# Optimization experiments

Measured on AMD Instinct MI355X. Metric: run time of the kernel, lower is better.

## Reference

```python
import jax, jax.numpy as jnp
import numpy as np

D_MODEL = 1024
NUM_HEADS = 16
MAX_SEQ_LEN = 2048
THETA = 10000.0
HEAD_DIM = D_MODEL // NUM_HEADS  # 64


def _trunc_normal(key, shape, std):
    # truncated normal in [-3, 3] sigma, matching nn.init.trunc_normal_
    return std * jax.random.truncated_normal(key, -3.0, 3.0, shape, dtype=jnp.float32)


def setup_inputs() -> dict:
    key = jax.random.key(0)
    kx, kq, kk, kv, ko = jax.random.split(key, 5)
    B, L = 2, 2048
    sigma = np.sqrt(2.0 / (D_MODEL + D_MODEL))
    x = jax.random.normal(kx, (B, L, D_MODEL), dtype=jnp.float32)
    token_positions = jnp.arange(L, dtype=jnp.int64 if jax.config.jax_enable_x64 else jnp.int32)[None, :]
    return {
        "x": x,
        "wq": _trunc_normal(kq, (D_MODEL, D_MODEL), sigma),
        "wk": _trunc_normal(kk, (D_MODEL, D_MODEL), sigma),
        "wv": _trunc_normal(kv, (D_MODEL, D_MODEL), sigma),
        "wo": _trunc_normal(ko, (D_MODEL, D_MODEL), sigma),
        "token_positions": token_positions,
    }


def _rope_tables():
    pos = jnp.arange(MAX_SEQ_LEN, dtype=jnp.float32)
    d_idx = jnp.arange(HEAD_DIM // 2, dtype=jnp.float32)
    inv_freq = THETA ** (-2.0 * d_idx / HEAD_DIM)
    angles = pos[:, None] * inv_freq[None, :]  # [max_seq_len, head_dim/2]
    return jnp.cos(angles), jnp.sin(angles)


def _apply_rope(x, cos, sin):
    # x: [b, n, l, h]; cos/sin: [1, l, h/2] (broadcast over b, n)
    xe = x[..., 0::2]
    xo = x[..., 1::2]
    oe = cos * xe - sin * xo
    oo = sin * xe + cos * xo
    # interleave back: stack last axis then flatten pairs
    out = jnp.stack([oe, oo], axis=-1)
    return out.reshape(x.shape)


def reference(x, wq, wk, wv, wo, token_positions):
    B, L, _ = x.shape
    cos_t, sin_t = _rope_tables()
    cos = cos_t[token_positions]  # [1, L, h/2]
    sin = sin_t[token_positions]

    def proj(w):
        y = jnp.einsum('bld,ed->ble', x, w)
        return y.reshape(B, L, NUM_HEADS, HEAD_DIM).transpose(0, 2, 1, 3)  # b n l h

    q, k, v = proj(wq), proj(wk), proj(wv)
    q = _apply_rope(q, cos, sin)
    k = _apply_rope(k, cos, sin)

    scale = 1.0 / np.sqrt(HEAD_DIM).astype(np.float32)
    logits = jnp.einsum('bnqh,bnkh->bnqk', q, k) * scale
    causal = jnp.tril(jnp.ones((L, L), dtype=bool))
    logits = jnp.where(causal[None, None], logits, -jnp.inf)
    scores = jax.nn.softmax(logits, axis=-1)
    out = jnp.einsum('bnqk,bnkh->bnqh', scores, v)
    out = out.transpose(0, 2, 1, 3).reshape(B, L, D_MODEL)
    return jnp.einsum('bld,ed->ble', out, wo)
```

## Files before the change

kernel.cpp:

```cpp
#include <hip/hip_runtime.h>
#include <stdint.h>
#include <stddef.h>

#define SEQ   2048
#define HD    64
#define DM    1024
#define NHEAD 16

typedef __bf16 bf16x8 __attribute__((ext_vector_type(8)));
typedef __bf16 bf16x4 __attribute__((ext_vector_type(4)));
typedef float  f32x4  __attribute__((ext_vector_type(4)));
typedef uint32_t u32x2 __attribute__((ext_vector_type(2)));
typedef uint32_t u32x4 __attribute__((ext_vector_type(4)));

#define MFMA16x16(a, b, c) __builtin_amdgcn_mfma_f32_16x16x32_bf16((a), (b), (c), 0, 0, 0)

__device__ __forceinline__ void gload16(const void* g, void* lds_uniform) {
    __builtin_amdgcn_global_load_lds(
        (const __attribute__((address_space(1))) uint32_t*)g,
        (__attribute__((address_space(3))) uint32_t*)lds_uniform, 16, 0, 0);
}

__global__ void prep_kernel(const float* __restrict__ x,
                            const float* __restrict__ wq, const float* __restrict__ wk,
                            const float* __restrict__ wv, const float* __restrict__ wo,
                            __bf16* __restrict__ xb, __bf16* __restrict__ wqkv,
                            __bf16* __restrict__ wob, float2* __restrict__ ctst) {
    int bid = blockIdx.x;
    if (bid < 4096) {
        int i = (bid * 256 + threadIdx.x) * 4;
        const float4 v = *(const float4*)(x + i);
        __bf16 o[4] = {(__bf16)v.x, (__bf16)v.y, (__bf16)v.z, (__bf16)v.w};
        *(uint64_t*)(xb + i) = *(const uint64_t*)o;
    } else if (bid < 8192) {
        int g = (bid - 4096) >> 10;
        int i = (((bid - 4096) & 1023) * 256 + threadIdx.x) * 4;
        const float* src = (g == 0) ? wq : (g == 1) ? wk : (g == 2) ? wv : wo;
        __bf16* dst = (g == 3) ? wob : (wqkv + (size_t)g * 1048576);
        const float4 v = *(const float4*)(src + i);
        __bf16 o[4] = {(__bf16)v.x, (__bf16)v.y, (__bf16)v.z, (__bf16)v.w};
        *(uint64_t*)(dst + i) = *(const uint64_t*)o;
    } else {
        int i = (bid - 8192) * 256 + threadIdx.x;
        int p = i & 31;
        int pos = i >> 5;
        float freq = expf(-(float)p * (logf(10000.0f) / 32.0f));
        float ang = (float)pos * freq;
        ctst[i] = make_float2(cosf(ang), sinf(ang));
    }
}

template <int MODE, int BN, int WPEU>
__global__ __launch_bounds__(256, WPEU)
void gemm_bt_kernel(const __bf16* __restrict__ A, const __bf16* __restrict__ W,
                    float* __restrict__ C, __bf16* __restrict__ Qb,
                    __bf16* __restrict__ Kb, __bf16* __restrict__ VTb,
                    const int* __restrict__ tpos, const float2* __restrict__ ctst,
                    int N, int K) {
    constexpr int NJ = BN >> 5;
    __shared__ __align__(16) char smem[16384 + BN * 128];
    char* As = smem;
    char* Bs = smem + 16384;
    const int lane = threadIdx.x & 63;
    const int w    = threadIdx.x >> 6;

    const int nbn = N / BN;
    const int per = (nbn * 32) >> 3;
    const int id  = blockIdx.x;
    const int lin = (id & 7) * per + (id >> 3);
    const int bm  = lin / nbn;
    const int bn  = lin % nbn;

    const int rbase = (w >> 1) * 64;
    const int cbase = (w & 1) * (BN / 2);

    f32x4 acc[4][NJ] = {};

    const int kt_iters = K >> 6;
    for (int kt = 0; kt < kt_iters; ++kt) {
        #pragma unroll
        for (int c = 0; c < 4; ++c) {
            int id2 = (c * 4 + w) * 64 + lane;
            int row = id2 >> 3, cc = id2 & 7;
            int koff = kt * 64 + ((cc ^ (row & 7)) << 3);
            gload16(A + (size_t)(bm * 128 + row) * K + koff, As + (c * 4 + w) * 1024);
        }
        #pragma unroll
        for (int c = 0; c < NJ; ++c) {
            int id2 = (c * 4 + w) * 64 + lane;
            int row = id2 >> 3, cc = id2 & 7;
            int koff = kt * 64 + ((cc ^ (row & 7)) << 3);
            gload16(W + (size_t)(bn * BN + row) * K + koff, Bs + (c * 4 + w) * 1024);
        }
        __syncthreads();
        #pragma unroll
        for (int ks = 0; ks < 2; ++ks) {
            bf16x8 af[4], bfr[NJ];
            #pragma unroll
            for (int i = 0; i < 4; ++i) {
                int row = rbase + i * 16 + (lane & 15);
                int c = ks * 4 + (lane >> 4);
                af[i] = *(const bf16x8*)(As + row * 128 + ((c ^ (row & 7)) << 4));
            }
            #pragma unroll
            for (int j = 0; j < NJ; ++j) {
                int row = cbase + j * 16 + (lane & 15);
                int c = ks * 4 + (lane >> 4);
                bfr[j] = *(const bf16x8*)(Bs + row * 128 + ((c ^ (row & 7)) << 4));
            }
            #pragma unroll
            for (int i = 0; i < 4; ++i)
                #pragma unroll
                for (int j = 0; j < NJ; ++j)
                    acc[i][j] = MFMA16x16(af[i], bfr[j], acc[i][j]);
        }
        __syncthreads();
    }

    if (MODE == 1) {
        #pragma unroll
        for (int i = 0; i < 4; ++i)
            #pragma unroll
            for (int j = 0; j < NJ; ++j)
                #pragma unroll
                for (int r = 0; r < 4; ++r) {
                    int m = bm * 128 + rbase + i * 16 + (lane >> 4) * 4 + r;
                    int n = bn * BN + cbase + j * 16 + (lane & 15);
                    C[(size_t)m * N + n] = acc[i][j][r];
                }
    } else {
        const int which = bn >> 3;
        char* T = smem + w * 8192;
        #pragma unroll
        for (int i = 0; i < 4; ++i)
            #pragma unroll
            for (int j = 0; j < NJ; ++j)
                #pragma unroll
                for (int r = 0; r < 4; ++r) {
                    int mi = i * 16 + (lane >> 4) * 4 + r;
                    int ni = j * 16 + (lane & 15);
                    __bf16 v = (__bf16)acc[i][j][r];
                    if (which == 2)
                        *(__bf16*)(T + ni * 128 + ((mi * 2) ^ ((ni & 7) << 4))) = v;
                    else
                        *(__bf16*)(T + mi * 128 + ((ni * 2) ^ ((mi & 7) << 4))) = v;
                }
        #pragma unroll
        for (int it = 0; it < 8; ++it) {
            int id2 = it * 64 + lane;
            int row = id2 >> 3, cc = id2 & 7;
            bf16x8 v = *(const bf16x8*)(T + row * 128 + ((cc ^ (row & 7)) << 4));
            if (which == 2) {
                int n = bn * BN + cbase + row;
                int m = bm * 128 + rbase + cc * 8;
                int b = m >> 11, l = m & (SEQ - 1);
                int h = (n & (DM - 1)) >> 6, d = n & 63;
                *(bf16x8*)(VTb + ((size_t)((b * NHEAD + h) * HD + d) * SEQ) + l) = v;
            } else {
                int m = bm * 128 + rbase + row;
                int n = bn * BN + cbase + cc * 8;
                int b = m >> 11, l = m & (SEQ - 1);
                int h = (n & (DM - 1)) >> 6, d = n & 63;
                int pb = tpos[l] * 32 + (d >> 1);
                float sc = (which == 0) ? 0.18033688011112042f : 1.0f;
                bf16x8 ov;
                #pragma unroll
                for (int jj = 0; jj < 4; ++jj) {
                    float2 cs = ctst[pb + jj];
                    float e = (float)v[2 * jj], dd = (float)v[2 * jj + 1];
                    ov[2 * jj]     = (__bf16)(sc * (cs.x * e - cs.y * dd));
                    ov[2 * jj + 1] = (__bf16)(sc * (cs.y * e + cs.x * dd));
                }
                __bf16* dst = which ? Kb : Qb;
                *(bf16x8*)(dst + ((size_t)(b * NHEAD + h) * SEQ + l) * HD + d) = ov;
            }
        }
    }
}

__global__ __launch_bounds__(256, 4)
void attn_kernel(const __bf16* __restrict__ Q, const __bf16* __restrict__ K,
                 const __bf16* __restrict__ VT, __bf16* __restrict__ O) {
    __shared__ __align__(16) char smem[32768];
    const int lane = threadIdx.x & 63;
    const int w    = threadIdx.x >> 6;
    const int tid  = threadIdx.x;
    const int hi   = lane >> 4;
    const int lo   = lane & 15;

    const int bid = blockIdx.x;
    const int xcd = bid & 7;
    const int idx = bid >> 3;
    const int s   = idx & 31;
    const int r   = idx >> 5;
    const int bh  = xcd * 4 + r;
    const int qb  = (r & 1) ? s : (31 - s);

    const __bf16* Qbh  = Q  + (size_t)bh * SEQ * HD;
    const __bf16* Kbh  = K  + (size_t)bh * SEQ * HD;
    const __bf16* VTbh = VT + (size_t)bh * HD * SEQ;
    const int b = bh >> 4, h = bh & 15;

    {
        #pragma unroll
        for (int c = 0; c < 2; ++c) {
            int id = c * 256 + tid;
            int row = id >> 3, cc = id & 7;
            int sw = (cc ^ (row & 7)) << 3;
            gload16(Kbh + (size_t)row * HD + sw, smem + (c * 4 + w) * 1024);
        }
        #pragma unroll
        for (int c = 0; c < 2; ++c) {
            int id = c * 256 + tid;
            int row = id >> 3, cc = id & 7;
            int jA = ((cc >> 2) << 5) | ((cc & 3) << 2);
            u32x2 a = *(const u32x2*)(VTbh + (size_t)row * SEQ + jA);
            u32x2 bq = *(const u32x2*)(VTbh + (size_t)row * SEQ + jA + 16);
            u32x4 v4 = {a[0], a[1], bq[0], bq[1]};
            *(u32x4*)(smem + 8192 + row * 128 + ((cc ^ (row & 7)) << 4)) = v4;
        }
    }

    const int qrow = qb * 64 + w * 16 + lo;
    bf16x8 qf[2];
    qf[0] = *(const bf16x8*)(Qbh + (size_t)qrow * HD + hi * 8);
    qf[1] = *(const bf16x8*)(Qbh + (size_t)qrow * HD + 32 + hi * 8);

    bf16x8 ones;
    #pragma unroll
    for (int i = 0; i < 8; ++i) ones[i] = (__bf16)1.0f;

    f32x4 o[4] = {};
    f32x4 ls = {};

    int cur = 0;
    __syncthreads();

    for (int kb = 0; kb <= qb; ++kb) {
        bf16x8 kreg[2];
        u32x4  vreg[2];
        if (kb < qb) {
            #pragma unroll
            for (int c = 0; c < 2; ++c) {
                int id = c * 256 + tid;
                int row = id >> 3, cc = id & 7;
                kreg[c] = *(const bf16x8*)(Kbh + (size_t)((kb + 1) * 64 + row) * HD + cc * 8);
                int jA = ((cc >> 2) << 5) | ((cc & 3) << 2);
                const __bf16* vsrc = VTbh + (size_t)row * SEQ + (kb + 1) * 64 + jA;
                u32x2 a = *(const u32x2*)(vsrc);
                u32x2 bq = *(const u32x2*)(vsrc + 16);
                vreg[c] = u32x4{a[0], a[1], bq[0], bq[1]};
            }
        }

        char* Ks = smem + cur * 16384;
        char* Vs = Ks + 8192;

        f32x4 s4[4];
        __builtin_amdgcn_s_setprio(1);
        #pragma unroll
        for (int jt = 0; jt < 4; ++jt) {
            f32x4 z = {};
            #pragma unroll
            for (int ks = 0; ks < 2; ++ks) {
                int row = jt * 16 + lo;
                int c = ks * 4 + hi;
                bf16x8 kf = *(const bf16x8*)(Ks + row * 128 + ((c ^ (row & 7)) << 4));
                z = MFMA16x16(kf, qf[ks], z);
            }
            s4[jt] = z;
        }
        __builtin_amdgcn_s_setprio(0);

        if (kb == qb) {
            int i = qb * 64 + w * 16 + lo;
            #pragma unroll
            for (int jt = 0; jt < 4; ++jt)
                #pragma unroll
                for (int rr = 0; rr < 4; ++rr) {
                    int j = kb * 64 + jt * 16 + hi * 4 + rr;
                    if (j > i) s4[jt][rr] = -1e30f;
                }
        }

        bf16x8 pk8[2];
        #pragma unroll
        for (int js = 0; js < 2; ++js)
            #pragma unroll
            for (int e = 0; e < 8; ++e)
                pk8[js][e] = (__bf16)exp2f(s4[2 * js + (e >> 2)][e & 3] - 16.0f);

        __builtin_amdgcn_s_setprio(1);
        #pragma unroll
        for (int js = 0; js < 2; ++js) {
            ls = MFMA16x16(pk8[js], ones, ls);
            int cb = js * 4 + hi;
            #pragma unroll
            for (int dt = 0; dt < 4; ++dt) {
                int vrow = dt * 16 + lo;
                bf16x8 vf = *(const bf16x8*)(Vs + vrow * 128 + ((cb ^ (vrow & 7)) << 4));
                o[dt] = MFMA16x16(pk8[js], vf, o[dt]);
            }
        }
        __builtin_amdgcn_s_setprio(0);

        if (kb < qb) {
            char* Kn = smem + (cur ^ 1) * 16384;
            char* Vn = Kn + 8192;
            #pragma unroll
            for (int c = 0; c < 2; ++c) {
                int id = c * 256 + tid;
                int row = id >> 3, cc = id & 7;
                int sw = (cc ^ (row & 7)) << 4;
                *(bf16x8*)(Kn + row * 128 + sw) = kreg[c];
                *(u32x4*)(Vn + row * 128 + sw) = vreg[c];
            }
        }

        __syncthreads();
        cur ^= 1;
    }

    float linv[4];
    #pragma unroll
    for (int rr = 0; rr < 4; ++rr) linv[rr] = 1.0f / ls[rr];

    char* Os = smem;
    #pragma unroll
    for (int dt = 0; dt < 4; ++dt)
        #pragma unroll
        for (int rr = 0; rr < 4; ++rr) {
            int orow = w * 16 + hi * 4 + rr;
            int oc = (dt * 16 + lo) * 2;
            *(__bf16*)(Os + orow * 128 + (oc ^ ((orow & 7) << 4))) = (__bf16)(o[dt][rr] * linv[rr]);
        }
    __syncthreads();

    #pragma unroll
    for (int c = 0; c < 2; ++c) {
        int id = c * 256 + tid;
        int row = id >> 3, cc = id & 7;
        bf16x8 v = *(const bf16x8*)(Os + row * 128 + ((cc ^ (row & 7)) << 4));
        *(bf16x8*)(O + (size_t)(b * SEQ + qb * 64 + row) * DM + h * HD + cc * 8) = v;
    }
}

extern "C" void kernel_launch(void* const* d_in, const int* in_sizes, int n_in,
                              void* d_out, int out_size, void* d_ws, size_t ws_size,
                              hipStream_t stream) {
    const float* x  = (const float*)d_in[0];
    const float* wq = (const float*)d_in[1];
    const float* wk = (const float*)d_in[2];
    const float* wv = (const float*)d_in[3];
    const float* wo = (const float*)d_in[4];
    const int* tpos = (const int*)d_in[5];
    float* out = (float*)d_out;
    char* ws = (char*)d_ws;

    __bf16* xb   = (__bf16*)(ws);
    __bf16* wqkv = (__bf16*)(ws + (size_t)(8  << 20));
    __bf16* wob  = (__bf16*)(ws + (size_t)(14 << 20));
    __bf16* Qb   = (__bf16*)(ws + (size_t)(16 << 20));
    __bf16* Kb   = (__bf16*)(ws + (size_t)(24 << 20));
    __bf16* VTb  = (__bf16*)(ws + (size_t)(32 << 20));
    __bf16* Ob   = (__bf16*)(ws + (size_t)(40 << 20));
    float2* ctst = (float2*)(ws + (size_t)(48 << 20));

    prep_kernel<<<8448, 256, 0, stream>>>(x, wq, wk, wv, wo, xb, wqkv, wob, ctst);
    gemm_bt_kernel<0, 128, 3><<<768, 256, 0, stream>>>(xb, wqkv, nullptr, Qb, Kb, VTb,
                                                       tpos, ctst, 3072, 1024);
    attn_kernel<<<1024, 256, 0, stream>>>(Qb, Kb, VTb, Ob);
    gemm_bt_kernel<1, 64, 4><<<512, 256, 0, stream>>>(Ob, wob, out, nullptr, nullptr, nullptr,
                                                      nullptr, nullptr, 1024, 1024);
}
```

Before: 99.79 us.

## Software-pipeline attention loop: overlap next QK^T with current PV and exp

```diff
diff --git a/kernel.cpp b/kernel.cpp
--- a/kernel.cpp
+++ b/kernel.cpp
@@ -226,6 +226,22 @@
     qf[0] = *(const bf16x8*)(Qbh + (size_t)qrow * HD + hi * 8);
     qf[1] = *(const bf16x8*)(Qbh + (size_t)qrow * HD + 32 + hi * 8);
 
+    bf16x8 kreg[2];
+    u32x4  vreg[2];
+    if (qb > 0) {
+        #pragma unroll
+        for (int c = 0; c < 2; ++c) {
+            int id = c * 256 + tid;
+            int row = id >> 3, cc = id & 7;
+            kreg[c] = *(const bf16x8*)(Kbh + (size_t)(64 + row) * HD + cc * 8);
+            int jA = ((cc >> 2) << 5) | ((cc & 3) << 2);
+            const __bf16* vsrc = VTbh + (size_t)row * SEQ + 64 + jA;
+            u32x2 a = *(const u32x2*)(vsrc);
+            u32x2 bq = *(const u32x2*)(vsrc + 16);
+            vreg[c] = u32x4{a[0], a[1], bq[0], bq[1]};
+        }
+    }
+
     bf16x8 ones;
     #pragma unroll
     for (int i = 0; i < 8; ++i) ones[i] = (__bf16)1.0f;
@@ -236,27 +252,9 @@
     int cur = 0;
     __syncthreads();
 
-    for (int kb = 0; kb <= qb; ++kb) {
-        bf16x8 kreg[2];
-        u32x4  vreg[2];
-        if (kb < qb) {
-            #pragma unroll
-            for (int c = 0; c < 2; ++c) {
-                int id = c * 256 + tid;
-                int row = id >> 3, cc = id & 7;
-                kreg[c] = *(const bf16x8*)(Kbh + (size_t)((kb + 1) * 64 + row) * HD + cc * 8);
-                int jA = ((cc >> 2) << 5) | ((cc & 3) << 2);
-                const __bf16* vsrc = VTbh + (size_t)row * SEQ + (kb + 1) * 64 + jA;
-                u32x2 a = *(const u32x2*)(vsrc);
-                u32x2 bq = *(const u32x2*)(vsrc + 16);
-                vreg[c] = u32x4{a[0], a[1], bq[0], bq[1]};
-            }
-        }
-
-        char* Ks = smem + cur * 16384;
-        char* Vs = Ks + 8192;
-
-        f32x4 s4[4];
+    f32x4 s4[4];
+    {
+        char* Ks = smem;
         __builtin_amdgcn_s_setprio(1);
         #pragma unroll
         for (int jt = 0; jt < 4; ++jt) {
@@ -271,39 +269,9 @@
             s4[jt] = z;
         }
         __builtin_amdgcn_s_setprio(0);
-
-        if (kb == qb) {
-            int i = qb * 64 + w * 16 + lo;
-            #pragma unroll
-            for (int jt = 0; jt < 4; ++jt)
-                #pragma unroll
-                for (int rr = 0; rr < 4; ++rr) {
-                    int j = kb * 64 + jt * 16 + hi * 4 + rr;
-                    if (j > i) s4[jt][rr] = -1e30f;
-                }
-        }
-
-        bf16x8 pk8[2];
-        #pragma unroll
-        for (int js = 0; js < 2; ++js)
-            #pragma unroll
-            for (int e = 0; e < 8; ++e)
-                pk8[js][e] = (__bf16)exp2f(s4[2 * js + (e >> 2)][e & 3] - 16.0f);
-
-        __builtin_amdgcn_s_setprio(1);
-        #pragma unroll
-        for (int js = 0; js < 2; ++js) {
-            ls = MFMA16x16(pk8[js], ones, ls);
-            int cb = js * 4 + hi;
-            #pragma unroll
-            for (int dt = 0; dt < 4; ++dt) {
-                int vrow = dt * 16 + lo;
-                bf16x8 vf = *(const bf16x8*)(Vs + vrow * 128 + ((cb ^ (vrow & 7)) << 4));
-                o[dt] = MFMA16x16(pk8[js], vf, o[dt]);
-            }
-        }
-        __builtin_amdgcn_s_setprio(0);
-
+    }
+
+    for (int kb = 0; kb <= qb; ++kb) {
         if (kb < qb) {
             char* Kn = smem + (cur ^ 1) * 16384;
             char* Vn = Kn + 8192;
@@ -315,6 +283,71 @@
                 *(bf16x8*)(Kn + row * 128 + sw) = kreg[c];
                 *(u32x4*)(Vn + row * 128 + sw) = vreg[c];
             }
+        }
+
+        if (kb == qb) {
+            int i16 = w * 16 + lo;
+            #pragma unroll
+            for (int jt = 0; jt < 4; ++jt)
+                #pragma unroll
+                for (int rr = 0; rr < 4; ++rr)
+                    if (jt * 16 + hi * 4 + rr > i16) s4[jt][rr] = -1e30f;
+        }
+        bf16x8 pk8[2];
+        #pragma unroll
+        for (int js = 0; js < 2; ++js)
+            #pragma unroll
+            for (int e = 0; e < 8; ++e)
+                pk8[js][e] = (__bf16)exp2f(s4[2 * js + (e >> 2)][e & 3] - 16.0f);
+
+        if (kb + 1 < qb) {
+            #pragma unroll
+            for (int c = 0; c < 2; ++c) {
+                int id = c * 256 + tid;
+                int row = id >> 3, cc = id & 7;
+                kreg[c] = *(const bf16x8*)(Kbh + (size_t)((kb + 2) * 64 + row) * HD + cc * 8);
+                int jA = ((cc >> 2) << 5) | ((cc & 3) << 2);
+                const __bf16* vsrc = VTbh + (size_t)row * SEQ + (kb + 2) * 64 + jA;
+                u32x2 a = *(const u32x2*)(vsrc);
+                u32x2 bq = *(const u32x2*)(vsrc + 16);
+                vreg[c] = u32x4{a[0], a[1], bq[0], bq[1]};
+            }
+        }
+
+        if (kb < qb) {
+            __syncthreads();
+            char* Ksn = smem + (cur ^ 1) * 16384;
+            __builtin_amdgcn_s_setprio(1);
+            #pragma unroll
+            for (int jt = 0; jt < 4; ++jt) {
+                f32x4 z = {};
+                #pragma unroll
+                for (int ks = 0; ks < 2; ++ks) {
+                    int row = jt * 16 + lo;
+                    int c = ks * 4 + hi;
+                    bf16x8 kf = *(const bf16x8*)(Ksn + row * 128 + ((c ^ (row & 7)) << 4));
+                    z = MFMA16x16(kf, qf[ks], z);
+                }
+                s4[jt] = z;
+            }
+            __builtin_amdgcn_s_setprio(0);
+        }
+
+        {
+            char* Vs = smem + cur * 16384 + 8192;
+            __builtin_amdgcn_s_setprio(1);
+            #pragma unroll
+            for (int js = 0; js < 2; ++js) {
+                ls = MFMA16x16(pk8[js], ones, ls);
+                int cb = js * 4 + hi;
+                #pragma unroll
+                for (int dt = 0; dt < 4; ++dt) {
+                    int vrow = dt * 16 + lo;
+                    bf16x8 vf = *(const bf16x8*)(Vs + vrow * 128 + ((cb ^ (vrow & 7)) << 4));
+                    o[dt] = MFMA16x16(pk8[js], vf, o[dt]);
+                }
+            }
+            __builtin_amdgcn_s_setprio(0);
         }
 
         __syncthreads();
```

Result: no change. 99.70 us (-0.1%).
